# Optimization experiments

Hardware: AMD Instinct MI355X
Metric: run time of the kernel (lower is better)

Reference implementation:

```python
import jax, jax.numpy as jnp
import numpy as np

B, T, FB, C = 2, 256, 128, 128
H_T, H_F, BAND = 4, 4, 16
INNER = 4 * C


def setup_inputs() -> dict:
    key = jax.random.key(0)
    ks = jax.random.split(key, 8)
    g = lambda k, shp: jax.random.normal(k, shp, jnp.float32) * 0.02
    return {
        "x": jax.random.normal(ks[0], (B, T, FB, C), jnp.float32),
        # temporal pre-norm + MHA (in_proj [3C,C], out_proj [C,C])
        "ln_t_w": jnp.ones((C,), jnp.float32), "ln_t_b": jnp.zeros((C,), jnp.float32),
        "t_wi": g(ks[1], (3 * C, C)), "t_bi": jnp.zeros((3 * C,), jnp.float32),
        "t_wo": g(ks[2], (C, C)), "t_bo": jnp.zeros((C,), jnp.float32),
        # frequency pre-norm + MHA
        "ln_f_w": jnp.ones((C,), jnp.float32), "ln_f_b": jnp.zeros((C,), jnp.float32),
        "f_wi": g(ks[3], (3 * C, C)), "f_bi": jnp.zeros((3 * C,), jnp.float32),
        "f_wo": g(ks[4], (C, C)), "f_bo": jnp.zeros((C,), jnp.float32),
        # FFN pre-norm + two linears
        "ln_n_w": jnp.ones((C,), jnp.float32), "ln_n_b": jnp.zeros((C,), jnp.float32),
        "w1": g(ks[5], (INNER, C)), "b1": jnp.zeros((INNER,), jnp.float32),
        "w2": g(ks[6], (C, INNER)), "b2": jnp.zeros((C,), jnp.float32),
    }


def _ln(x, w, b, eps=1e-5):
    mu = x.mean(-1, keepdims=True)
    var = ((x - mu) ** 2).mean(-1, keepdims=True)
    return (x - mu) * jax.lax.rsqrt(var + eps) * w + b


def _mha(x, wi, bi, wo, bo, h, mask):
    """torch.nn.MultiheadAttention equivalent. x: [..., S, C], mask: additive [S, S]."""
    c = x.shape[-1]
    dh = c // h
    qkv = x @ wi.T + bi
    q, k, v = jnp.split(qkv, 3, axis=-1)
    split = lambda t: t.reshape(t.shape[:-1] + (h, dh)).swapaxes(-2, -3)  # [..., h, S, dh]
    q, k, v = split(q), split(k), split(v)
    scores = jnp.einsum('...hqd,...hkd->...hqk', q, k) * (1.0 / np.sqrt(dh)) + mask
    attn = jax.nn.softmax(scores, axis=-1)
    o = jnp.einsum('...hqk,...hkd->...hqd', attn, v)
    o = o.swapaxes(-2, -3).reshape(x.shape)
    return o @ wo.T + bo


def _causal_mask(n):
    i = jnp.arange(n)
    return jnp.where(i[:, None] >= i[None, :], 0.0, -jnp.inf).astype(jnp.float32)


def _band_mask(n, band):
    i = jnp.arange(n)
    return jnp.where(jnp.abs(i[:, None] - i[None, :]) <= band, 0.0, -jnp.inf).astype(jnp.float32)


def reference(x, ln_t_w, ln_t_b, t_wi, t_bi, t_wo, t_bo,
              ln_f_w, ln_f_b, f_wi, f_bi, f_wo, f_bo,
              ln_n_w, ln_n_b, w1, b1, w2, b2):
    cm = _causal_mask(x.shape[1])      # [T, T]
    bm = _band_mask(x.shape[2], BAND)  # [F, F]
    # temporal causal MHSA per frequency bin (pre-norm residual)
    xt = _ln(x, ln_t_w, ln_t_b).transpose(0, 2, 1, 3)  # [B, F, T, C]
    x = x + _mha(xt, t_wi, t_bi, t_wo, t_bo, H_T, cm).transpose(0, 2, 1, 3)
    # banded local MHSA over frequency per time step
    xf = _ln(x, ln_f_w, ln_f_b)  # [B, T, F, C]
    x = x + _mha(xf, f_wi, f_bi, f_wo, f_bo, H_F, bm)
    # FFN (Linear -> exact GELU -> Linear)
    xn = _ln(x, ln_n_w, ln_n_b)
    h = jax.nn.gelu(xn @ w1.T + b1, approximate=False)
    x = x + (h @ w2.T + b2)
    return x
```

## Files before the change

kernel.cpp:

```cpp
#include <hip/hip_runtime.h>
#include <math.h>

typedef __bf16 bf16;
typedef __bf16 bf16x8 __attribute__((ext_vector_type(8)));
typedef __bf16 bf16x4 __attribute__((ext_vector_type(4)));
typedef __bf16 bf16x2 __attribute__((ext_vector_type(2)));
typedef float f32x4 __attribute__((ext_vector_type(4)));
typedef float f32x2 __attribute__((ext_vector_type(2)));
typedef float f32x16 __attribute__((ext_vector_type(16)));
typedef unsigned int u32;
typedef unsigned int u32x4 __attribute__((ext_vector_type(4)));

#define AS1 __attribute__((address_space(1)))
#define AS3 __attribute__((address_space(3)))

static __device__ __forceinline__ f32x4 mfma16(bf16x8 a, bf16x8 b, f32x4 c) {
    return __builtin_amdgcn_mfma_f32_16x16x32_bf16(a, b, c, 0, 0, 0);
}
static __device__ __forceinline__ f32x16 mfma32(bf16x8 a, bf16x8 b, f32x16 c) {
    return __builtin_amdgcn_mfma_f32_32x32x16_bf16(a, b, c, 0, 0, 0);
}
static __device__ __forceinline__ u32 pk2(float a, float b) {
    bf16x2 v; v[0] = (bf16)a; v[1] = (bf16)b;
    return __builtin_bit_cast(u32, v);
}
static __device__ __forceinline__ float gelu_f(float x) {
    float u = 0.7978845608f * x * __builtin_fmaf(0.044715f, x * x, 1.0f);
    float e = __expf(2.0f * u);
    return x - x * __builtin_amdgcn_rcpf(e + 1.0f);
}

__global__ __launch_bounds__(256) void cvt_w6(
    const float* __restrict__ s0, const float* __restrict__ s1,
    const float* __restrict__ s2, const float* __restrict__ s3,
    const float* __restrict__ s4, const float* __restrict__ s5,
    bf16* __restrict__ dst)
{
    int i = (blockIdx.x * 256 + threadIdx.x) * 4;
    const float* src; int off;
    if      (i <  49152) { src = s0; off = 0; }
    else if (i <  65536) { src = s1; off = 49152; }
    else if (i < 114688) { src = s2; off = 65536; }
    else if (i < 131072) { src = s3; off = 114688; }
    else if (i < 196608) { src = s4; off = 131072; }
    else                 { src = s5; off = 196608; }
    f32x4 v = *(const f32x4*)&src[i - off];
    bf16x4 b;
    b[0] = (bf16)v[0]; b[1] = (bf16)v[1]; b[2] = (bf16)v[2]; b[3] = (bf16)v[3];
    *(bf16x4*)&dst[i] = b;
}

template<int OUT_BF16, int RES, int RESBF, int GELU_, int LNA, int KT, int NT>
__global__ __launch_bounds__(256) void gemm_rw(
    const bf16* __restrict__ A, const bf16* __restrict__ W,
    const float* __restrict__ bias, const void* __restrict__ res,
    void* __restrict__ outp,
    const float* __restrict__ xf, const float* __restrict__ lnaw,
    const float* __restrict__ lnab)
{
    constexpr int N = NT * 128;
    __shared__ __align__(16) bf16 Bs[128 * 64];
    const int tid  = threadIdx.x;
    const int lane = tid & 63;
    const int w    = tid >> 6;
    const int li = lane & 15, g = lane >> 4;
    const int m0 = blockIdx.x * 64;
    const int arow = m0 + w * 16 + li;
    const bf16* ap = A + (size_t)arow * KT;

    bf16x8 afrag[4];
    if constexpr (LNA) {
        int b = arow >> 15, f = (arow >> 8) & 127, t = arow & 255;
        const float* xp = xf + (((size_t)b * 256 + t) * 128 + f) * 128;
        f32x4 cv[8];
        #pragma unroll
        for (int cc = 0; cc < 4; ++cc) {
            cv[2 * cc]     = *(const f32x4*)&xp[cc * 32 + g * 8];
            cv[2 * cc + 1] = *(const f32x4*)&xp[cc * 32 + g * 8 + 4];
        }
        float sm = 0.f, sq = 0.f;
        #pragma unroll
        for (int i = 0; i < 8; ++i)
            #pragma unroll
            for (int j = 0; j < 4; ++j) { float v = cv[i][j]; sm += v; sq += v * v; }
        sm += __shfl_xor(sm, 16); sm += __shfl_xor(sm, 32);
        sq += __shfl_xor(sq, 16); sq += __shfl_xor(sq, 32);
        float mu = sm * 0.0078125f;
        float rs = rsqrtf(sq * 0.0078125f - mu * mu + 1e-5f);
        #pragma unroll
        for (int cc = 0; cc < 4; ++cc) {
            f32x4 w0 = *(const f32x4*)&lnaw[cc * 32 + g * 8];
            f32x4 w1 = *(const f32x4*)&lnaw[cc * 32 + g * 8 + 4];
            f32x4 b0 = *(const f32x4*)&lnab[cc * 32 + g * 8];
            f32x4 b1 = *(const f32x4*)&lnab[cc * 32 + g * 8 + 4];
            #pragma unroll
            for (int j = 0; j < 4; ++j) {
                afrag[cc][j]     = (bf16)((cv[2 * cc][j]     - mu) * rs * w0[j] + b0[j]);
                afrag[cc][4 + j] = (bf16)((cv[2 * cc + 1][j] - mu) * rs * w1[j] + b1[j]);
            }
        }
    } else if constexpr (KT == 128) {
        #pragma unroll
        for (int cc = 0; cc < 4; ++cc)
            afrag[cc] = *(const bf16x8*)&ap[cc * 32 + g * 8];
    }

    #pragma unroll
    for (int t = 0; t < NT; ++t) {
        const int n0 = t * 128;
        f32x4 acc[8] = {};

        #pragma unroll
        for (int k0 = 0; k0 < KT; k0 += 64) {
            #pragma unroll
            for (int it = 0; it < 4; ++it) {
                int idx = it * 256 + tid;
                int brow = idx >> 3, bch = idx & 7;
                const bf16* gp = W + (size_t)(n0 + brow) * KT + k0 + ((bch ^ (brow & 7)) * 8);
                __builtin_amdgcn_global_load_lds((AS1 void*)gp, (AS3 void*)(Bs + idx * 8), 16, 0, 0);
            }
            bf16x8 av0, av1;
            if constexpr (KT != 128) {
                av0 = *(const bf16x8*)&ap[k0 + g * 8];
                av1 = *(const bf16x8*)&ap[k0 + 32 + g * 8];
            }
            __syncthreads();
            #pragma unroll
            for (int kk = 0; kk < 2; ++kk) {
                bf16x8 av;
                if constexpr (KT == 128) av = afrag[(k0 >> 5) + kk];
                else                     av = kk ? av1 : av0;
                #pragma unroll
                for (int j = 0; j < 8; ++j) {
                    int brow = j * 16 + li;
                    int bch = (kk * 4 + g) ^ (li & 7);
                    bf16x8 bv = *(const bf16x8*)&Bs[brow * 64 + bch * 8];
                    acc[j] = mfma16(av, bv, acc[j]);
                }
            }
            __syncthreads();
        }

        float bcol[8];
        #pragma unroll
        for (int j = 0; j < 8; ++j) bcol[j] = bias[n0 + j * 16 + li];

        const int row0 = m0 + w * 16 + g * 4;
        #pragma unroll
        for (int r = 0; r < 4; ++r) {
            int row = row0 + r;
            #pragma unroll
            for (int j = 0; j < 8; ++j) {
                size_t off = (size_t)row * N + n0 + j * 16 + li;
                float v = acc[j][r] + bcol[j];
                if constexpr (RES) {
                    if constexpr (RESBF) v += (float)((const bf16*)res)[off];
                    else                 v += ((const float*)res)[off];
                }
                if constexpr (GELU_) v = gelu_f(v);
                if constexpr (OUT_BF16) ((bf16*)outp)[off] = (bf16)v;
                else                    ((float*)outp)[off] = v;
            }
        }
    }
}

template<int MODE, int RESBF>
__global__ __launch_bounds__(256) void attn_fused(
    const bf16* __restrict__ qkv, const bf16* __restrict__ Wo,
    const float* __restrict__ bo, const void* __restrict__ res,
    bf16* __restrict__ xc, bf16* __restrict__ xn,
    const float* __restrict__ lnw, const float* __restrict__ lnb)
{
    constexpr int S = (MODE == 0) ? 256 : 128;
    __shared__ __align__(16) bf16 o_lds[32 * 136];
    __shared__ float red[32][4][2];
    const int lane = threadIdx.x & 63;
    const int w = threadIdx.x >> 6;
    const int hi = lane >> 5;
    const int q31 = lane & 31;
    const int s = blockIdx.x;
    const int qb = blockIdx.y * 32;
    const int q = qb + q31;

    const size_t base = (size_t)s * S * 384;
    const bf16* qp = qkv + base + w * 32;
    const bf16* kp = qp + 128;
    const bf16* vp = qp + 256 + q31;

    bf16x8 qf0 = *(const bf16x8*)&qp[(size_t)q * 384 + hi * 8];
    bf16x8 qf1 = *(const bf16x8*)&qp[(size_t)q * 384 + 16 + hi * 8];

    f32x16 O = {};
    float m = -1e30f, l = 0.f;

    int klo, khi;
    if constexpr (MODE == 0) { klo = 0; khi = qb + 32; }
    else {
        klo = (qb > 16 ? (qb - 16) : 0) & ~31;
        khi = (qb + 48 < S) ? (qb + 48) : S;
    }

    const float sc = 0.17677669529663687f;

    for (int k0 = klo; k0 < khi; k0 += 32) {
        bf16x8 kf0 = *(const bf16x8*)&kp[(size_t)(k0 + q31) * 384 + hi * 8];
        bf16x8 kf1 = *(const bf16x8*)&kp[(size_t)(k0 + q31) * 384 + 16 + hi * 8];
        bf16x8 vf1, vf2;
        #pragma unroll
        for (int e = 0; e < 8; ++e) {
            vf1[e] = vp[(size_t)(k0 + hi * 8 + e) * 384];
            vf2[e] = vp[(size_t)(k0 + 16 + hi * 8 + e) * 384];
        }

        f32x16 st = {};
        st = mfma32(kf0, qf0, st);
        st = mfma32(kf1, qf1, st);

        float mx = -3.0e38f;
        #pragma unroll
        for (int r = 0; r < 16; ++r) {
            int krow = k0 + (r & 3) + 8 * (r >> 2) + 4 * hi;
            bool ok;
            if constexpr (MODE == 0) ok = (krow <= q);
            else { int d = krow - q; ok = (d <= 16 && d >= -16); }
            float v = ok ? st[r] * sc : -3.0e38f;
            st[r] = v;
            mx = fmaxf(mx, v);
        }
        mx = fmaxf(mx, __shfl_xor(mx, 32));
        float mn = fmaxf(m, mx);
        float resc = __expf(m - mn);
        m = mn;
        float ps = 0.f;
        #pragma unroll
        for (int r = 0; r < 16; ++r) {
            float p = __expf(st[r] - mn);
            st[r] = p;
            ps += p;
        }
        ps += __shfl_xor(ps, 32);
        l = l * resc + ps;
        #pragma unroll
        for (int r = 0; r < 16; ++r) O[r] *= resc;

        u32 c01 = pk2(st[0], st[1]),   c23 = pk2(st[2], st[3]);
        u32 c45 = pk2(st[4], st[5]),   c67 = pk2(st[6], st[7]);
        u32 c89 = pk2(st[8], st[9]),   cAB = pk2(st[10], st[11]);
        u32 cCD = pk2(st[12], st[13]), cEF = pk2(st[14], st[15]);
        u32 x01 = __shfl_xor((int)c01, 32), x23 = __shfl_xor((int)c23, 32);
        u32 x45 = __shfl_xor((int)c45, 32), x67 = __shfl_xor((int)c67, 32);
        u32 x89 = __shfl_xor((int)c89, 32), xAB = __shfl_xor((int)cAB, 32);
        u32 xCD = __shfl_xor((int)cCD, 32), xEF = __shfl_xor((int)cEF, 32);
        u32x4 b1w = hi ? u32x4{x45, x67, c45, c67} : u32x4{c01, c23, x01, x23};
        u32x4 b2w = hi ? u32x4{xCD, xEF, cCD, cEF} : u32x4{c89, cAB, x89, xAB};
        bf16x8 B1 = __builtin_bit_cast(bf16x8, b1w);
        bf16x8 B2 = __builtin_bit_cast(bf16x8, b2w);

        O = mfma32(vf1, B1, O);
        O = mfma32(vf2, B2, O);
    }

    float inv = 1.f / l;
    #pragma unroll
    for (int mb = 0; mb < 4; ++mb) {
        bf16x4 ov;
        #pragma unroll
        for (int j = 0; j < 4; ++j) ov[j] = (bf16)(O[mb * 4 + j] * inv);
        *(bf16x4*)&o_lds[q31 * 136 + w * 32 + mb * 8 + hi * 4] = ov;
    }
    __syncthreads();

    const int li = lane & 15, g = lane >> 4;
    bf16x8 af[2][4];
    #pragma unroll
    for (int mi = 0; mi < 2; ++mi)
        #pragma unroll
        for (int kk = 0; kk < 4; ++kk)
            af[mi][kk] = *(const bf16x8*)&o_lds[(mi * 16 + li) * 136 + kk * 32 + g * 8];

    f32x4 acc[2][2] = {};
    #pragma unroll
    for (int ni = 0; ni < 2; ++ni) {
        #pragma unroll
        for (int kk = 0; kk < 4; ++kk) {
            bf16x8 bv = *(const bf16x8*)&Wo[(size_t)(w * 32 + ni * 16 + li) * 128 + kk * 32 + g * 8];
            acc[0][ni] = mfma16(af[0][kk], bv, acc[0][ni]);
            acc[1][ni] = mfma16(af[1][kk], bv, acc[1][ni]);
        }
    }

    int b0_ = 0, f0_ = 0;
    if constexpr (MODE == 0) { b0_ = s >> 7; f0_ = s & 127; }
    float vals[2][2][4];
    size_t groff[2][4];
    #pragma unroll
    for (int mi = 0; mi < 2; ++mi) {
        #pragma unroll
        for (int r = 0; r < 4; ++r) {
            int mrow = qb + mi * 16 + g * 4 + r;
            size_t orow;
            if constexpr (MODE == 0) orow = ((size_t)(b0_ * 256 + mrow)) * 128 + f0_;
            else                     orow = (size_t)s * 128 + mrow;
            groff[mi][r] = orow * 128;
            #pragma unroll
            for (int ni = 0; ni < 2; ++ni) {
                int col = w * 32 + ni * 16 + li;
                float v = acc[mi][ni][r] + bo[col];
                if constexpr (RESBF) v += (float)((const bf16*)res)[groff[mi][r] + col];
                else                 v += ((const float*)res)[groff[mi][r] + col];
                vals[mi][ni][r] = v;
            }
        }
    }
    #pragma unroll
    for (int mi = 0; mi < 2; ++mi) {
        #pragma unroll
        for (int r = 0; r < 4; ++r) {
            float sm = vals[mi][0][r] + vals[mi][1][r];
            float sq = vals[mi][0][r] * vals[mi][0][r] + vals[mi][1][r] * vals[mi][1][r];
            #pragma unroll
            for (int off = 1; off < 16; off <<= 1) {
                sm += __shfl_xor(sm, off);
                sq += __shfl_xor(sq, off);
            }
            if (li == 0) {
                red[mi * 16 + g * 4 + r][w][0] = sm;
                red[mi * 16 + g * 4 + r][w][1] = sq;
            }
        }
    }
    __syncthreads();
    #pragma unroll
    for (int mi = 0; mi < 2; ++mi) {
        #pragma unroll
        for (int r = 0; r < 4; ++r) {
            int mrow = mi * 16 + g * 4 + r;
            f32x4 p0 = *(const f32x4*)&red[mrow][0][0];
            f32x4 p1 = *(const f32x4*)&red[mrow][2][0];
            float smt = p0[0] + p0[2] + p1[0] + p1[2];
            float sqt = p0[1] + p0[3] + p1[1] + p1[3];
            float mu = smt * 0.0078125f;
            float rs = rsqrtf(sqt * 0.0078125f - mu * mu + 1e-5f);
            #pragma unroll
            for (int ni = 0; ni < 2; ++ni) {
                int col = w * 32 + ni * 16 + li;
                float v = vals[mi][ni][r];
                xc[groff[mi][r] + col] = (bf16)v;
                xn[groff[mi][r] + col] = (bf16)((v - mu) * rs * lnw[col] + lnb[col]);
            }
        }
    }
}

extern "C" void kernel_launch(void* const* d_in, const int* in_sizes, int n_in,
                              void* d_out, int out_size, void* d_ws, size_t ws_size,
                              hipStream_t stream) {
    const float* x      = (const float*)d_in[0];
    const float* ln_t_w = (const float*)d_in[1];
    const float* ln_t_b = (const float*)d_in[2];
    const float* t_wi   = (const float*)d_in[3];
    const float* t_bi   = (const float*)d_in[4];
    const float* t_wo   = (const float*)d_in[5];
    const float* t_bo   = (const float*)d_in[6];
    const float* ln_f_w = (const float*)d_in[7];
    const float* ln_f_b = (const float*)d_in[8];
    const float* f_wi   = (const float*)d_in[9];
    const float* f_bi   = (const float*)d_in[10];
    const float* f_wo   = (const float*)d_in[11];
    const float* f_bo   = (const float*)d_in[12];
    const float* ln_n_w = (const float*)d_in[13];
    const float* ln_n_b = (const float*)d_in[14];
    const float* w1     = (const float*)d_in[15];
    const float* b1     = (const float*)d_in[16];
    const float* w2     = (const float*)d_in[17];
    const float* b2     = (const float*)d_in[18];

    char* ws = (char*)d_ws;
    bf16* wbf  = (bf16*)ws;
    bf16* xn   = (bf16*)(ws + 524288);
    bf16* qkvh = (bf16*)(ws + 524288 + 16777216);
    bf16* xcA  = (bf16*)(ws + 524288 + 16777216 + 67108864 + 16777216);
    bf16* xcB  = (bf16*)(ws + 524288 + 16777216 + 67108864 + 2 * 16777216);
    float* out = (float*)d_out;

    const bf16* twi_b = wbf + 0;
    const bf16* two_b = wbf + 49152;
    const bf16* fwi_b = wbf + 65536;
    const bf16* fwo_b = wbf + 114688;
    const bf16* w1_b  = wbf + 131072;
    const bf16* w2_b  = wbf + 196608;

    cvt_w6<<<256, 256, 0, stream>>>(t_wi, t_wo, f_wi, f_wo, w1, w2, wbf);

    gemm_rw<1, 0, 0, 0, 1, 128, 3><<<1024, 256, 0, stream>>>(
        nullptr, twi_b, t_bi, nullptr, qkvh, x, ln_t_w, ln_t_b);
    attn_fused<0, 0><<<dim3(256, 8), 256, 0, stream>>>(
        qkvh, two_b, t_bo, x, xcA, xn, ln_f_w, ln_f_b);

    gemm_rw<1, 0, 0, 0, 0, 128, 3><<<1024, 256, 0, stream>>>(
        xn, fwi_b, f_bi, nullptr, qkvh, nullptr, nullptr, nullptr);
    attn_fused<1, 1><<<dim3(512, 4), 256, 0, stream>>>(
        qkvh, fwo_b, f_bo, xcA, xcB, xn, ln_n_w, ln_n_b);

    gemm_rw<1, 0, 0, 1, 0, 128, 4><<<1024, 256, 0, stream>>>(
        xn, w1_b, b1, nullptr, qkvh, nullptr, nullptr, nullptr);
    gemm_rw<0, 1, 1, 0, 0, 512, 1><<<1024, 256, 0, stream>>>(
        qkvh, w2_b, b2, xcB, out, nullptr, nullptr, nullptr);

    (void)in_sizes; (void)n_in; (void)out_size; (void)ws_size;
}
```

Baseline: 165.9 us.

## Store temporal-attention outputs in sequence order and gather rows in frequency GEMM

The temporal attention kernel now writes its residual and normalized outputs contiguously in [B,F,T] order rather than scattering them into [B,T,F]. The frequency QKV GEMM remaps its A-row index to read from that layout, and the frequency attention reads its residual with the matching permuted index. Separately, Q is pre-scaled by the softmax scale before the loop, and mask evaluation is skipped for fully unmasked causal blocks. The intent is to cut scattered global stores and per-score ALU work; the trade-off is strided gathers in the GEMM A loads and slightly different rounding from scaling Q in bf16.

```diff
diff --git a/kernel.cpp b/kernel.cpp
--- a/kernel.cpp
+++ b/kernel.cpp
@@ -50,7 +50,7 @@
     *(bf16x4*)&dst[i] = b;
 }
 
-template<int OUT_BF16, int RES, int RESBF, int GELU_, int LNA, int KT, int NT>
+template<int OUT_BF16, int RES, int RESBF, int GELU_, int LNA, int RMAP, int KT, int NT>
 __global__ __launch_bounds__(256) void gemm_rw(
     const bf16* __restrict__ A, const bf16* __restrict__ W,
     const float* __restrict__ bias, const void* __restrict__ res,
@@ -66,7 +66,12 @@
     const int li = lane & 15, g = lane >> 4;
     const int m0 = blockIdx.x * 64;
     const int arow = m0 + w * 16 + li;
-    const bf16* ap = A + (size_t)arow * KT;
+    int srow = arow;
+    if constexpr (RMAP) {
+        int b = arow >> 15, t = (arow >> 7) & 255, f = arow & 127;
+        srow = (b << 15) + (f << 8) + t;
+    }
+    const bf16* ap = A + (size_t)srow * KT;
 
     bf16x8 afrag[4];
     if constexpr (LNA) {
@@ -188,8 +193,15 @@
     const bf16* kp = qp + 128;
     const bf16* vp = qp + 256 + q31;
 
-    bf16x8 qf0 = *(const bf16x8*)&qp[(size_t)q * 384 + hi * 8];
-    bf16x8 qf1 = *(const bf16x8*)&qp[(size_t)q * 384 + 16 + hi * 8];
+    const float sc = 0.17677669529663687f;
+    bf16x8 qr0 = *(const bf16x8*)&qp[(size_t)q * 384 + hi * 8];
+    bf16x8 qr1 = *(const bf16x8*)&qp[(size_t)q * 384 + 16 + hi * 8];
+    bf16x8 qf0, qf1;
+    #pragma unroll
+    for (int e = 0; e < 8; ++e) {
+        qf0[e] = (bf16)((float)qr0[e] * sc);
+        qf1[e] = (bf16)((float)qr1[e] * sc);
+    }
 
     f32x16 O = {};
     float m = -1e30f, l = 0.f;
@@ -201,8 +213,6 @@
         khi = (qb + 48 < S) ? (qb + 48) : S;
     }
 
-    const float sc = 0.17677669529663687f;
-
     for (int k0 = klo; k0 < khi; k0 += 32) {
         bf16x8 kf0 = *(const bf16x8*)&kp[(size_t)(k0 + q31) * 384 + hi * 8];
         bf16x8 kf1 = *(const bf16x8*)&kp[(size_t)(k0 + q31) * 384 + 16 + hi * 8];
@@ -217,17 +227,19 @@
         st = mfma32(kf0, qf0, st);
         st = mfma32(kf1, qf1, st);
 
-        float mx = -3.0e38f;
-        #pragma unroll
-        for (int r = 0; r < 16; ++r) {
-            int krow = k0 + (r & 3) + 8 * (r >> 2) + 4 * hi;
-            bool ok;
-            if constexpr (MODE == 0) ok = (krow <= q);
-            else { int d = krow - q; ok = (d <= 16 && d >= -16); }
-            float v = ok ? st[r] * sc : -3.0e38f;
-            st[r] = v;
-            mx = fmaxf(mx, v);
-        }
+        if (MODE == 1 || k0 + 32 > qb) {
+            #pragma unroll
+            for (int r = 0; r < 16; ++r) {
+                int krow = k0 + (r & 3) + 8 * (r >> 2) + 4 * hi;
+                bool ok;
+                if constexpr (MODE == 0) ok = (krow <= q);
+                else { int d = krow - q; ok = (d <= 16 && d >= -16); }
+                st[r] = ok ? st[r] : -3.0e38f;
+            }
+        }
+        float mx = st[0];
+        #pragma unroll
+        for (int r = 1; r < 16; ++r) mx = fmaxf(mx, st[r]);
         mx = fmaxf(mx, __shfl_xor(mx, 32));
         float mn = fmaxf(m, mx);
         float resc = __expf(m - mn);
@@ -290,25 +302,26 @@
         }
     }
 
-    int b0_ = 0, f0_ = 0;
-    if constexpr (MODE == 0) { b0_ = s >> 7; f0_ = s & 127; }
     float vals[2][2][4];
-    size_t groff[2][4];
     #pragma unroll
     for (int mi = 0; mi < 2; ++mi) {
         #pragma unroll
         for (int r = 0; r < 4; ++r) {
-            int mrow = qb + mi * 16 + g * 4 + r;
-            size_t orow;
-            if constexpr (MODE == 0) orow = ((size_t)(b0_ * 256 + mrow)) * 128 + f0_;
-            else                     orow = (size_t)s * 128 + mrow;
-            groff[mi][r] = orow * 128;
+            int lr = qb + mi * 16 + g * 4 + r;
+            size_t rrow;
+            if constexpr (MODE == 0) {
+                int b = s >> 7, f = s & 127;
+                rrow = ((size_t)(b * 256 + lr)) * 128 + f;
+            } else {
+                int b = s >> 8, t = s & 255;
+                rrow = (size_t)b * 32768 + (size_t)lr * 256 + t;
+            }
             #pragma unroll
             for (int ni = 0; ni < 2; ++ni) {
                 int col = w * 32 + ni * 16 + li;
                 float v = acc[mi][ni][r] + bo[col];
-                if constexpr (RESBF) v += (float)((const bf16*)res)[groff[mi][r] + col];
-                else                 v += ((const float*)res)[groff[mi][r] + col];
+                if constexpr (RESBF) v += (float)((const bf16*)res)[rrow * 128 + col];
+                else                 v += ((const float*)res)[rrow * 128 + col];
                 vals[mi][ni][r] = v;
             }
         }
@@ -342,12 +355,13 @@
             float sqt = p0[1] + p0[3] + p1[1] + p1[3];
             float mu = smt * 0.0078125f;
             float rs = rsqrtf(sqt * 0.0078125f - mu * mu + 1e-5f);
+            size_t woff = ((size_t)s * S + qb + mrow) * 128;
             #pragma unroll
             for (int ni = 0; ni < 2; ++ni) {
                 int col = w * 32 + ni * 16 + li;
                 float v = vals[mi][ni][r];
-                xc[groff[mi][r] + col] = (bf16)v;
-                xn[groff[mi][r] + col] = (bf16)((v - mu) * rs * lnw[col] + lnb[col]);
+                xc[woff + col] = (bf16)v;
+                xn[woff + col] = (bf16)((v - mu) * rs * lnw[col] + lnb[col]);
             }
         }
     }
@@ -393,19 +407,19 @@
 
     cvt_w6<<<256, 256, 0, stream>>>(t_wi, t_wo, f_wi, f_wo, w1, w2, wbf);
 
-    gemm_rw<1, 0, 0, 0, 1, 128, 3><<<1024, 256, 0, stream>>>(
+    gemm_rw<1, 0, 0, 0, 1, 0, 128, 3><<<1024, 256, 0, stream>>>(
         nullptr, twi_b, t_bi, nullptr, qkvh, x, ln_t_w, ln_t_b);
     attn_fused<0, 0><<<dim3(256, 8), 256, 0, stream>>>(
         qkvh, two_b, t_bo, x, xcA, xn, ln_f_w, ln_f_b);
 
-    gemm_rw<1, 0, 0, 0, 0, 128, 3><<<1024, 256, 0, stream>>>(
+    gemm_rw<1, 0, 0, 0, 0, 1, 128, 3><<<1024, 256, 0, stream>>>(
         xn, fwi_b, f_bi, nullptr, qkvh, nullptr, nullptr, nullptr);
     attn_fused<1, 1><<<dim3(512, 4), 256, 0, stream>>>(
         qkvh, fwo_b, f_bo, xcA, xcB, xn, ln_n_w, ln_n_b);
 
-    gemm_rw<1, 0, 0, 1, 0, 128, 4><<<1024, 256, 0, stream>>>(
+    gemm_rw<1, 0, 0, 1, 0, 0, 128, 4><<<1024, 256, 0, stream>>>(
         xn, w1_b, b1, nullptr, qkvh, nullptr, nullptr, nullptr);
-    gemm_rw<0, 1, 1, 0, 0, 512, 1><<<1024, 256, 0, stream>>>(
+    gemm_rw<0, 1, 1, 0, 0, 0, 512, 1><<<1024, 256, 0, stream>>>(
         qkvh, w2_b, b2, xcB, out, nullptr, nullptr, nullptr);
 
     (void)in_sizes; (void)n_in; (void)out_size; (void)ws_size;
```

Measured after the change: 166.8 us. No clear change (+0.5%).
